# Kernel tuning notes

Hardware: AMD Instinct MI355X
Metric: run time of the kernel (lower is better)

## Reference

```python
import jax, jax.numpy as jnp
import numpy as np

B, T, C, H = 8, 1024, 1024, 16
HD = C // H  # head dim = 64
NEG = -1e9


def setup_inputs() -> dict:
    key = jax.random.key(0)
    ks = jax.random.split(key, 10)
    total = B * T
    x = jax.random.normal(ks[0], (total, C), dtype=jnp.float32)
    # identity pack: each padded row is a contiguous chunk of tokens
    padpack_index = jnp.arange(total, dtype=jnp.int64).reshape(B, T)
    # sorted per-row sequence ids -> block-diagonal attention within each packed row
    padpack_batch = jnp.sort(jax.random.randint(ks[1], (B, T), 0, 4, dtype=jnp.int32), axis=-1)
    padpack_inverse_index = jnp.arange(total, dtype=jnp.int64)
    s = 1.0 / np.sqrt(C)
    Wq = jax.random.uniform(ks[2], (C, C), jnp.float32, -s, s)
    bq = jax.random.uniform(ks[3], (C,), jnp.float32, -s, s)
    Wk = jax.random.uniform(ks[4], (C, C), jnp.float32, -s, s)
    bk = jax.random.uniform(ks[5], (C,), jnp.float32, -s, s)
    Wv = jax.random.uniform(ks[6], (C, C), jnp.float32, -s, s)
    bv = jax.random.uniform(ks[7], (C,), jnp.float32, -s, s)
    Wp = jax.random.uniform(ks[8], (C, C), jnp.float32, -s, s)
    bp = jax.random.uniform(ks[9], (C,), jnp.float32, -s, s)
    return {"x": x, "padpack_index": padpack_index, "padpack_batch": padpack_batch,
            "padpack_inverse_index": padpack_inverse_index,
            "Wq": Wq, "bq": bq, "Wk": Wk, "bk": bk, "Wv": Wv, "bv": bv, "Wp": Wp, "bp": bp}


def reference(x, padpack_index, padpack_batch, padpack_inverse_index,
              Wq, bq, Wk, bk, Wv, bv, Wp, bp):
    # gather ragged tokens into padded [B, T, C]
    xp = x[padpack_index]
    # torch Linear: y = x @ W.T + b
    q = (xp @ Wq.T + bq).reshape(B, T, H, HD)
    k = (xp @ Wk.T + bk).reshape(B, T, H, HD)
    v = (xp @ Wv.T + bv).reshape(B, T, H, HD)
    scale = 1.0 / np.sqrt(HD).astype(np.float32)
    att = jnp.einsum('bihd,bjhd->bhij', q, k) * scale  # [B,H,T,T]
    # mask: token pairs from different packed sequences cannot attend
    mask = (padpack_batch[:, :, None] != padpack_batch[:, None, :])[:, None]  # [B,1,T,T]
    att = jnp.where(mask, NEG, att)
    att = jax.nn.softmax(att, axis=-1)
    y = jnp.einsum('bhij,bjhd->bihd', att, v).reshape(B, T, C)
    y = y @ Wp.T + bp
    # scatter back to ragged layout [total_tokens, C]
    return y.reshape(B * T, C)[padpack_inverse_index]
```

## Files before the change

### kernel.cpp

```cpp
#include <hip/hip_runtime.h>


typedef __attribute__((ext_vector_type(8))) short short8;
typedef __attribute__((ext_vector_type(4))) float f32x4;

#define MFMA16(a, b, c) __builtin_amdgcn_mfma_f32_16x16x32_bf16((a), (b), (c), 0, 0, 0)

__device__ __forceinline__ ushort f2b(float f) {
  union { float f; unsigned u; } v; v.f = f;
  unsigned u = v.u;
  return (ushort)((u + 0x7fffu + ((u >> 16) & 1u)) >> 16);
}

__device__ __forceinline__ void gload16(const void* g, void* l) {
  __builtin_amdgcn_global_load_lds((const __attribute__((address_space(1))) unsigned int*)g,
                                   (__attribute__((address_space(3))) unsigned int*)l,
                                   16, 0, 0);
}

__device__ __forceinline__ void cvt4(const float* __restrict__ s, ushort* __restrict__ d) {
  const float4 v = *(const float4*)s;
  ushort4 r; r.x = f2b(v.x); r.y = f2b(v.y); r.z = f2b(v.z); r.w = f2b(v.w);
  *(ushort4*)d = r;
}

__global__ __launch_bounds__(256) void prep(const float* __restrict__ x,
    const float* __restrict__ wq, const float* __restrict__ wk,
    const float* __restrict__ wv, const float* __restrict__ wp,
    ushort* __restrict__ xb, ushort* __restrict__ wb) {
  const long long e0 = ((long long)blockIdx.x * 256 + threadIdx.x) * 4;
  const long long NX = 8388608ll;
  if (e0 < NX) {
    cvt4(x + e0, xb + e0);
  } else {
    const long long t = e0 - NX;
    const int sel = (int)(t >> 20);
    const float* w = sel == 0 ? wq : sel == 1 ? wk : sel == 2 ? wv : wp;
    cvt4(w + (t & 1048575), wb + t);
  }
}

__global__ void seg_bounds(const int* __restrict__ pb, int* __restrict__ bnd) {
  const int b = blockIdx.x, i = threadIdx.x;
  const int* p = pb + b * 1024;
  const int cur = p[i];
  const int prev = (i == 0) ? -1 : p[i - 1];
  for (int v = prev + 1; v <= cur; ++v) bnd[b * 8 + v] = i;
  if (i == 1023)
    for (int v = cur + 1; v <= 4; ++v) bnd[b * 8 + v] = 1024;
}

template <int MODE>
__global__ __launch_bounds__(512, 2) void gemm8(
    const ushort* __restrict__ A, const ushort* __restrict__ Bw,
    const float* __restrict__ bias0, const float* __restrict__ bias1,
    const float* __restrict__ bias2,
    ushort* __restrict__ O0, ushort* __restrict__ O1, ushort* __restrict__ O2,
    float* __restrict__ Of) {
  constexpr int ACH = 256 * 64;
  constexpr int BCH = 128 * 64;
  constexpr int BUFB = 2 * (ACH + BCH);
  __shared__ __align__(16) char smem[3 * BUFB];

  const int tid = threadIdx.x, lane = tid & 63, wid = tid >> 6;
  const int wr = wid >> 1, wc = wid & 1;
  const int lg = lane >> 4, lc = lane & 15;

  const int id = blockIdx.x;
  const int s = id >> 3;
  const int m0 = ((id & 7) * 4 + (s & 3)) << 8;
  const int n0 = (s >> 2) << 7;

  f32x4 acc[4][4] = {};

  const int sr0 = tid >> 2;
  const int sc0 = (tid & 3) ^ ((sr0 >> 1) & 3);

#define STAGE(dst_, kh, kt) { \
    char* ad = (dst_) + (kh) * ACH; \
    char* bd = (dst_) + 2 * ACH + (kh) * BCH; \
    const int kcol = (kt) * 64 + (kh) * 32; \
    gload16(A + (size_t)(m0 + sr0) * 1024 + kcol + sc0 * 8, ad + tid * 16); \
    gload16(A + (size_t)(m0 + 128 + sr0) * 1024 + kcol + sc0 * 8, ad + (tid + 512) * 16); \
    gload16(Bw + (size_t)(n0 + sr0) * 1024 + kcol + sc0 * 8, bd + tid * 16); \
  }

#define PHASE_COMPUTE(src_, kh) { \
    const char* ab = (src_) + (kh) * ACH; \
    const char* bb = (src_) + 2 * ACH + (kh) * BCH; \
    short8 af[4]; short8 bf[4]; \
    _Pragma("unroll") \
    for (int f = 0; f < 4; ++f) { \
      const int row = wr * 64 + f * 16 + lc; \
      af[f] = *(const short8*)(ab + row * 64 + ((lg ^ ((row >> 1) & 3)) << 4)); \
    } \
    _Pragma("unroll") \
    for (int g = 0; g < 4; ++g) { \
      const int row = wc * 64 + g * 16 + lc; \
      bf[g] = *(const short8*)(bb + row * 64 + ((lg ^ ((row >> 1) & 3)) << 4)); \
    } \
    asm volatile("s_waitcnt lgkmcnt(0)" ::: "memory"); \
    __builtin_amdgcn_sched_barrier(0); \
    __builtin_amdgcn_s_setprio(1); \
    _Pragma("unroll") \
    for (int f = 0; f < 4; ++f) \
      _Pragma("unroll") \
      for (int g = 0; g < 4; ++g) \
        acc[f][g] = MFMA16(af[f], bf[g], acc[f][g]); \
    __builtin_amdgcn_s_setprio(0); \
  }

#define WAITVM(n) { asm volatile("s_waitcnt vmcnt(" #n ")" ::: "memory"); }

  char* b0 = smem;
  char* b1 = smem + BUFB;
  char* b2 = smem + 2 * BUFB;

  STAGE(b0, 0, 0)
  STAGE(b0, 1, 0)
  STAGE(b1, 0, 1)
  STAGE(b1, 1, 1)

  for (int t = 0; t < 14; ++t) {
    WAITVM(9)
    __builtin_amdgcn_s_barrier();
    __builtin_amdgcn_sched_barrier(0);
    STAGE(b2, 0, t + 2)
    PHASE_COMPUTE(b0, 0)
    WAITVM(9)
    __builtin_amdgcn_s_barrier();
    __builtin_amdgcn_sched_barrier(0);
    STAGE(b2, 1, t + 2)
    PHASE_COMPUTE(b0, 1)
    char* tmp = b0; b0 = b1; b1 = b2; b2 = tmp;
  }
  WAITVM(9)
  __builtin_amdgcn_s_barrier();
  __builtin_amdgcn_sched_barrier(0);
  PHASE_COMPUTE(b0, 0)
  WAITVM(6)
  __builtin_amdgcn_s_barrier();
  __builtin_amdgcn_sched_barrier(0);
  PHASE_COMPUTE(b0, 1)
  WAITVM(3)
  __builtin_amdgcn_s_barrier();
  __builtin_amdgcn_sched_barrier(0);
  PHASE_COMPUTE(b1, 0)
  WAITVM(0)
  __builtin_amdgcn_s_barrier();
  __builtin_amdgcn_sched_barrier(0);
  PHASE_COMPUTE(b1, 1)

  if constexpr (MODE == 0) {
    const int sel = n0 >> 10, nloc = n0 & 1023;
    const float* bias = sel == 0 ? bias0 : sel == 1 ? bias1 : bias2;
    float bval[4];
#pragma unroll
    for (int g = 0; g < 4; ++g) bval[g] = bias[nloc + wc * 64 + g * 16 + lc];
    if (sel < 2) {
      ushort* dst = sel ? O1 : O0;
#pragma unroll
      for (int f = 0; f < 4; ++f)
#pragma unroll
        for (int j = 0; j < 4; ++j) {
          const size_t row = m0 + wr * 64 + f * 16 + lg * 4 + j;
#pragma unroll
          for (int g = 0; g < 4; ++g)
            dst[row * 1024 + nloc + wc * 64 + g * 16 + lc] = f2b(acc[f][g][j] + bval[g]);
        }
    } else {
      ushort (*Ts)[136] = (ushort(*)[136])smem;
#pragma unroll
      for (int mh = 0; mh < 2; ++mh) {
        __syncthreads();
        if ((wr >> 1) == mh) {
#pragma unroll
          for (int f = 0; f < 4; ++f)
#pragma unroll
            for (int g = 0; g < 4; ++g)
#pragma unroll
              for (int j = 0; j < 4; ++j)
                Ts[(wr & 1) * 64 + f * 16 + lg * 4 + j][wc * 64 + g * 16 + lc] =
                    f2b(acc[f][g][j] + bval[g]);
        }
        __syncthreads();
        const int c = tid >> 2;
        const int th = (tid & 3) * 32;
        const int gt = m0 + mh * 128;
        const int b = gt >> 10;
        const int t0 = (gt & 1023) + th;
        const int gc = nloc + c;
        ushort* dp = O2 + ((size_t)((b * 16 + (gc >> 6)) * 64 + (gc & 63))) * 1024 + t0;
#pragma unroll
        for (int gb = 0; gb < 4; ++gb) {
          short8 pk;
#pragma unroll
          for (int u = 0; u < 8; ++u) pk[u] = (short)Ts[th + gb * 8 + u][c];
          *(short8*)(dp + gb * 8) = pk;
        }
      }
    }
  } else {
    float bval[4];
#pragma unroll
    for (int g = 0; g < 4; ++g) bval[g] = bias0[n0 + wc * 64 + g * 16 + lc];
#pragma unroll
    for (int f = 0; f < 4; ++f)
#pragma unroll
      for (int j = 0; j < 4; ++j) {
        const size_t row = m0 + wr * 64 + f * 16 + lg * 4 + j;
#pragma unroll
        for (int g = 0; g < 4; ++g)
          Of[row * 1024 + n0 + wc * 64 + g * 16 + lc] = acc[f][g][j] + bval[g];
      }
  }
#undef STAGE
#undef PHASE_COMPUTE
#undef WAITVM
}

__global__ __launch_bounds__(256) void attn(const ushort* __restrict__ Q,
    const ushort* __restrict__ K, const ushort* __restrict__ Vt,
    const int* __restrict__ bnd, ushort* __restrict__ O) {
  __shared__ __align__(16) char kvbuf[2][16384];
  __shared__ __align__(16) ushort Plds[4][16][68];

  const int tid = threadIdx.x, lane = tid & 63, w = tid >> 6;
  const int lg = lane >> 4, lc = lane & 15;

  const int id = blockIdx.x;
  const int xcd = id & 7, slot = id >> 3;
  const int bh = xcd + 8 * (slot >> 4), qt = slot & 15;
  const int b = bh >> 4, h = bh & 15;
  const int q0 = qt * 64 + w * 16;

  const int* bd = bnd + b * 8;
  const int b1 = bd[1], b2 = bd[2], b3 = bd[3], b4 = bd[4];
#define SEGID(k) (((k) >= b1) + ((k) >= b2) + ((k) >= b3) + ((k) >= b4))

  const int qid = SEGID(q0 + lc);
  int klo_l = (qid > 0) ? b1 : 0;
  klo_l = (qid > 1) ? b2 : klo_l;
  klo_l = (qid > 2) ? b3 : klo_l;
  int khi_l = (qid > 0) ? b2 : b1;
  khi_l = (qid > 1) ? b3 : khi_l;
  khi_l = (qid > 2) ? b4 : khi_l;

  const int bq_lo = SEGID(qt * 64), bq_hi = SEGID(qt * 64 + 63);
  unsigned am = 0;
#pragma unroll
  for (int jt = 0; jt < 16; ++jt) {
    const int tlo = SEGID(jt * 64), thi = SEGID(jt * 64 + 63);
    if (thi >= bq_lo && tlo <= bq_hi) am |= (1u << jt);
  }

  const ushort* qp = Q + (size_t)(b * 1024 + q0 + lc) * 1024 + h * 64 + lg * 8;
  const short8 qf0 = *(const short8*)qp;
  const short8 qf1 = *(const short8*)(qp + 32);

  const int r0 = tid >> 3;
  const int c16 = (tid & 7) ^ (r0 & 7);
  const ushort* Kg0 = K + (size_t)(b * 1024 + r0) * 1024 + h * 64 + c16 * 8;
  const ushort* Kg1 = Kg0 + (size_t)32 * 1024;
  const ushort* Vg0 = Vt + (size_t)(bh * 64 + r0) * 1024 + c16 * 8;
  const ushort* Vg1 = Vg0 + (size_t)32 * 1024;

#define STAGE(bufp, j) { \
    gload16(Kg0 + (size_t)(j) * 1024, (bufp) + tid * 16); \
    gload16(Kg1 + (size_t)(j) * 1024, (bufp) + 4096 + tid * 16); \
    gload16(Vg0 + (j), (bufp) + 8192 + tid * 16); \
    gload16(Vg1 + (j), (bufp) + 12288 + tid * 16); }

#define SOFF(r, ch) ((r) * 128 + ((((ch) ^ ((r) & 7))) << 4))

  float mr = -1e30f, lr = 0.f;
  f32x4 o[4] = {};

  unsigned rem = am;
  int jc = __builtin_ctz(rem) * 64;
  rem &= rem - 1;
  STAGE(kvbuf[0], jc)
  __syncthreads();
  int cur = 0;

  for (;;) {
    int jn = -1;
    if (rem) {
      jn = __builtin_ctz(rem) * 64;
      rem &= rem - 1;
      STAGE(kvbuf[cur ^ 1], jn)
    }
    const char* bufK = kvbuf[cur];
    const char* bufV = kvbuf[cur] + 8192;

    short8 kf[8];
#pragma unroll
    for (int n = 0; n < 4; ++n) {
      const int rr = n * 16 + lc;
      kf[2 * n] = *(const short8*)(bufK + SOFF(rr, lg));
      kf[2 * n + 1] = *(const short8*)(bufK + SOFF(rr, lg + 4));
    }
    f32x4 s[4];
    __builtin_amdgcn_s_setprio(1);
#pragma unroll
    for (int n = 0; n < 4; ++n) {
      f32x4 z = {};
      z = MFMA16(kf[2 * n], qf0, z);
      s[n] = MFMA16(kf[2 * n + 1], qf1, z);
    }
    __builtin_amdgcn_s_setprio(0);

#pragma unroll
    for (int n = 0; n < 4; ++n) {
      const int kk = jc + n * 16 + lg * 4;
#pragma unroll
      for (int r = 0; r < 4; ++r) {
        const bool ok = (kk + r >= klo_l) && (kk + r < khi_l);
        s[n][r] = ok ? s[n][r] * 0.125f : -1e9f;
      }
    }

    float rm = fmaxf(fmaxf(fmaxf(s[0][0], s[0][1]), fmaxf(s[0][2], s[0][3])),
                     fmaxf(fmaxf(fmaxf(s[1][0], s[1][1]), fmaxf(s[1][2], s[1][3])),
                           fmaxf(fmaxf(fmaxf(s[2][0], s[2][1]), fmaxf(s[2][2], s[2][3])),
                                 fmaxf(fmaxf(s[3][0], s[3][1]), fmaxf(s[3][2], s[3][3])))));
    rm = fmaxf(rm, __shfl_xor(rm, 16));
    rm = fmaxf(rm, __shfl_xor(rm, 32));
    float mn = mr;
    if (!__all(rm <= mr + 8.f)) {
      mn = fmaxf(mr, rm);
      const float sf = __expf(mr - mn);
      mr = mn;
      lr *= sf;
      const float s0 = __shfl(sf, lg * 4 + 0);
      const float s1 = __shfl(sf, lg * 4 + 1);
      const float s2 = __shfl(sf, lg * 4 + 2);
      const float s3 = __shfl(sf, lg * 4 + 3);
#pragma unroll
      for (int n = 0; n < 4; ++n) {
        o[n][0] *= s0; o[n][1] *= s1; o[n][2] *= s2; o[n][3] *= s3;
      }
    }
    float rs = 0.f;
#pragma unroll
    for (int n = 0; n < 4; ++n)
#pragma unroll
      for (int r = 0; r < 4; ++r) {
        const float p = __expf(s[n][r] - mn);
        s[n][r] = p; rs += p;
      }
    rs += __shfl_xor(rs, 16);
    rs += __shfl_xor(rs, 32);
    lr += rs;

#pragma unroll
    for (int n = 0; n < 4; ++n) {
      ushort4 pk;
      pk.x = f2b(s[n][0]); pk.y = f2b(s[n][1]); pk.z = f2b(s[n][2]); pk.w = f2b(s[n][3]);
      *(ushort4*)&Plds[w][lc][n * 16 + lg * 4] = pk;
    }
    asm volatile("s_waitcnt lgkmcnt(0)" ::: "memory");
    __builtin_amdgcn_sched_barrier(0);
    const short8 p0 = *(const short8*)&Plds[w][lc][lg * 8];
    const short8 p1 = *(const short8*)&Plds[w][lc][32 + lg * 8];
    __builtin_amdgcn_sched_barrier(0);

    short8 vv[8];
#pragma unroll
    for (int n = 0; n < 4; ++n) {
      const int rr = n * 16 + lc;
      vv[2 * n] = *(const short8*)(bufV + SOFF(rr, lg));
      vv[2 * n + 1] = *(const short8*)(bufV + SOFF(rr, lg + 4));
    }
    __builtin_amdgcn_s_setprio(1);
#pragma unroll
    for (int n = 0; n < 4; ++n) {
      o[n] = MFMA16(p0, vv[2 * n], o[n]);
      o[n] = MFMA16(p1, vv[2 * n + 1], o[n]);
    }
    __builtin_amdgcn_s_setprio(0);

    if (jn < 0) break;
    __syncthreads();
    cur ^= 1;
    jc = jn;
  }

  const float linv = 1.f / lr;
  const float i0 = __shfl(linv, lg * 4 + 0);
  const float i1 = __shfl(linv, lg * 4 + 1);
  const float i2 = __shfl(linv, lg * 4 + 2);
  const float i3 = __shfl(linv, lg * 4 + 3);
#pragma unroll
  for (int n = 0; n < 4; ++n) {
    const size_t base = (size_t)(b * 1024 + q0) * 1024 + h * 64 + n * 16 + lc;
    O[base + 0 * 1024 + (size_t)lg * 4096] = f2b(o[n][0] * i0);
    O[base + 1 * 1024 + (size_t)lg * 4096] = f2b(o[n][1] * i1);
    O[base + 2 * 1024 + (size_t)lg * 4096] = f2b(o[n][2] * i2);
    O[base + 3 * 1024 + (size_t)lg * 4096] = f2b(o[n][3] * i3);
  }
#undef STAGE
#undef SOFF
#undef SEGID
}

extern "C" void kernel_launch(void* const* d_in, const int* in_sizes, int n_in,
                              void* d_out, int out_size, void* d_ws, size_t ws_size,
                              hipStream_t stream) {
  const float* x  = (const float*)d_in[0];
  const int*  pb  = (const int*)d_in[2];
  const float* Wq = (const float*)d_in[4]; const float* bq = (const float*)d_in[5];
  const float* Wk = (const float*)d_in[6]; const float* bk = (const float*)d_in[7];
  const float* Wv = (const float*)d_in[8]; const float* bv = (const float*)d_in[9];
  const float* Wp = (const float*)d_in[10]; const float* bp = (const float*)d_in[11];
  float* out = (float*)d_out;
  char* ws = (char*)d_ws;

  ushort* xb = (ushort*)ws;
  ushort* wb = (ushort*)(ws + (16u << 20));
  ushort* Qb = (ushort*)(ws + (24u << 20));
  ushort* Kb = (ushort*)(ws + (40u << 20));
  ushort* Vt = (ushort*)(ws + (56u << 20));
  int*    bnd = (int*)(ws + (72u << 20));
  ushort* Ob = xb;

  prep<<<12288, 256, 0, stream>>>(x, Wq, Wk, Wv, Wp, xb, wb);
  seg_bounds<<<8, 1024, 0, stream>>>(pb, bnd);
  gemm8<0><<<768, 512, 0, stream>>>(xb, wb, bq, bk, bv, Qb, Kb, Vt, nullptr);
  attn<<<2048, 256, 0, stream>>>(Qb, Kb, Vt, bnd, Ob);
  gemm8<1><<<256, 512, 0, stream>>>(Ob, wb + (3 << 20), bp,
                                    nullptr, nullptr, nullptr, nullptr, nullptr, out);
}
```

Before: 155.2 us.

## Add dedicated 256x256-tile QKV projection GEMM kernel with double-buffered LDS

Replaces the 256x128-tile QKV GEMM (768 blocks) with a new kernel that uses 256x256 output tiles (384 blocks), 8 waves in a 2x4 layout, each holding 8x4 MFMA accumulators. K is staged in 64-wide chunks through a double-buffered LDS pipeline using direct global-to-LDS loads, with setprio around MFMA bursts. The larger tile raises arithmetic intensity and cuts redundant A/B reloads, at the cost of more accumulator registers, 128KB LDS per block, and fewer blocks to spread across CUs. The old gemm8 is reduced to the output-projection mode only.

```diff
diff --git a/kernel.cpp b/kernel.cpp
--- a/kernel.cpp
+++ b/kernel.cpp
@@ -50,13 +50,175 @@
     for (int v = cur + 1; v <= 4; ++v) bnd[b * 8 + v] = 1024;
 }
 
+__global__ __launch_bounds__(512, 2) void gemm_qkv256(
+    const ushort* __restrict__ A, const ushort* __restrict__ Bw,
+    const float* __restrict__ bq, const float* __restrict__ bk, const float* __restrict__ bv,
+    ushort* __restrict__ Qb, ushort* __restrict__ Kb, ushort* __restrict__ Vt) {
+  constexpr int REG = 16384;
+  constexpr int BUFB = 4 * REG;
+  __shared__ __align__(16) char smem[2 * BUFB];
+
+  const int tid = threadIdx.x, lane = tid & 63, wid = tid >> 6;
+  const int wr = wid >> 2, wc = wid & 3;
+  const int lg = lane >> 4, lc = lane & 15;
+
+  const int id = blockIdx.x;
+  const int xcd = id & 7, s = id >> 3;
+  const int m0 = (xcd * 4 + (s & 3)) << 8;
+  const int n0 = (s >> 2) << 8;
+
+  f32x4 acc[8][4] = {};
+
+  const int sr = tid >> 2;
+  const int sc = (tid & 3) ^ ((sr >> 1) & 3);
+
+#define STG(bufp, reg_off, src, row_base, kcol) { \
+    gload16((src) + (size_t)((row_base) + sr) * 1024 + (kcol) + sc * 8, \
+            (bufp) + (reg_off) + tid * 16); \
+    gload16((src) + (size_t)((row_base) + 128 + sr) * 1024 + (kcol) + sc * 8, \
+            (bufp) + (reg_off) + 8192 + tid * 16); }
+
+#define RD_B(bufp, kh) { \
+    const char* bb = (bufp) + 2 * REG + (kh) * REG; \
+    _Pragma("unroll") \
+    for (int g = 0; g < 4; ++g) { \
+      const int row = wc * 64 + g * 16 + lc; \
+      bf[g] = *(const short8*)(bb + row * 64 + ((lg ^ ((row >> 1) & 3)) << 4)); \
+    } }
+
+#define RD_A(bufp, kh, mh) { \
+    const char* ab = (bufp) + (kh) * REG; \
+    _Pragma("unroll") \
+    for (int f = 0; f < 4; ++f) { \
+      const int row = wr * 128 + (mh) * 64 + f * 16 + lc; \
+      af[f] = *(const short8*)(ab + row * 64 + ((lg ^ ((row >> 1) & 3)) << 4)); \
+    } }
+
+#define DO_MFMA(mh) { \
+    asm volatile("s_waitcnt lgkmcnt(0)" ::: "memory"); \
+    __builtin_amdgcn_sched_barrier(0); \
+    __builtin_amdgcn_s_setprio(1); \
+    _Pragma("unroll") \
+    for (int f = 0; f < 4; ++f) \
+      _Pragma("unroll") \
+      for (int g = 0; g < 4; ++g) \
+        acc[(mh) * 4 + f][g] = MFMA16(af[f], bf[g], acc[(mh) * 4 + f][g]); \
+    __builtin_amdgcn_s_setprio(0); }
+
+#define BAR() { __builtin_amdgcn_s_barrier(); __builtin_amdgcn_sched_barrier(0); }
+#define WAITVM(n) { asm volatile("s_waitcnt vmcnt(" #n ")" ::: "memory"); }
+
+  char* cur = smem;
+  char* oth = smem + BUFB;
+
+  STG(cur, 0, A, m0, 0)
+  STG(cur, 2 * REG, Bw, n0, 0)
+  STG(cur, REG, A, m0, 32)
+  STG(cur, 3 * REG, Bw, n0, 32)
+
+  short8 af[4], bf[4];
+
+  for (int t = 0; t < 15; ++t) {
+    const int kn = (t + 1) * 64;
+    WAITVM(4)
+    BAR()
+    STG(oth, 0, A, m0, kn)
+    RD_B(cur, 0)
+    RD_A(cur, 0, 0)
+    DO_MFMA(0)
+    BAR()
+    STG(oth, 2 * REG, Bw, n0, kn)
+    RD_A(cur, 0, 1)
+    DO_MFMA(1)
+    WAITVM(4)
+    BAR()
+    STG(oth, REG, A, m0, kn + 32)
+    RD_B(cur, 1)
+    RD_A(cur, 1, 0)
+    DO_MFMA(0)
+    BAR()
+    STG(oth, 3 * REG, Bw, n0, kn + 32)
+    RD_A(cur, 1, 1)
+    DO_MFMA(1)
+    char* tmp = cur; cur = oth; oth = tmp;
+  }
+  WAITVM(4)
+  BAR()
+  RD_B(cur, 0)
+  RD_A(cur, 0, 0)
+  DO_MFMA(0)
+  BAR()
+  RD_A(cur, 0, 1)
+  DO_MFMA(1)
+  WAITVM(0)
+  BAR()
+  RD_B(cur, 1)
+  RD_A(cur, 1, 0)
+  DO_MFMA(0)
+  BAR()
+  RD_A(cur, 1, 1)
+  DO_MFMA(1)
+
+  const int sel = n0 >> 10, nloc = n0 & 1023;
+  const float* bias = sel == 0 ? bq : sel == 1 ? bk : bv;
+  float bval[4];
+#pragma unroll
+  for (int g = 0; g < 4; ++g) bval[g] = bias[nloc + wc * 64 + g * 16 + lc];
+
+  if (sel < 2) {
+    ushort* dst = sel ? Kb : Qb;
+#pragma unroll
+    for (int i = 0; i < 8; ++i)
+#pragma unroll
+      for (int j = 0; j < 4; ++j) {
+        const size_t row = m0 + wr * 128 + i * 16 + lg * 4 + j;
+#pragma unroll
+        for (int g = 0; g < 4; ++g)
+          dst[row * 1024 + nloc + wc * 64 + g * 16 + lc] = f2b(acc[i][g][j] + bval[g]);
+      }
+  } else {
+    ushort (*Ts)[264] = (ushort(*)[264])smem;
+#pragma unroll
+    for (int h2 = 0; h2 < 2; ++h2) {
+      __syncthreads();
+      if (wr == h2) {
+#pragma unroll
+        for (int i = 0; i < 8; ++i)
+#pragma unroll
+          for (int g = 0; g < 4; ++g)
+#pragma unroll
+            for (int j = 0; j < 4; ++j)
+              Ts[i * 16 + lg * 4 + j][wc * 64 + g * 16 + lc] = f2b(acc[i][g][j] + bval[g]);
+      }
+      __syncthreads();
+      const int c = tid >> 1;
+      const int th = (tid & 1) * 64;
+      const int gt = m0 + h2 * 128;
+      const int b = gt >> 10;
+      const int t0 = (gt & 1023) + th;
+      const int gc = nloc + c;
+      ushort* dp = Vt + ((size_t)((b * 16 + (gc >> 6)) * 64 + (gc & 63))) * 1024 + t0;
+#pragma unroll
+      for (int gb = 0; gb < 8; ++gb) {
+        short8 pk;
+#pragma unroll
+        for (int u = 0; u < 8; ++u) pk[u] = (short)Ts[th + gb * 8 + u][c];
+        *(short8*)(dp + gb * 8) = pk;
+      }
+    }
+  }
+#undef STG
+#undef RD_B
+#undef RD_A
+#undef DO_MFMA
+#undef BAR
+#undef WAITVM
+}
+
 template <int MODE>
 __global__ __launch_bounds__(512, 2) void gemm8(
     const ushort* __restrict__ A, const ushort* __restrict__ Bw,
-    const float* __restrict__ bias0, const float* __restrict__ bias1,
-    const float* __restrict__ bias2,
-    ushort* __restrict__ O0, ushort* __restrict__ O1, ushort* __restrict__ O2,
-    float* __restrict__ Of) {
+    const float* __restrict__ bias0, float* __restrict__ Of) {
   constexpr int ACH = 256 * 64;
   constexpr int BCH = 128 * 64;
   constexpr int BUFB = 2 * (ACH + BCH);
@@ -151,69 +313,18 @@
   __builtin_amdgcn_sched_barrier(0);
   PHASE_COMPUTE(b1, 1)
 
-  if constexpr (MODE == 0) {
-    const int sel = n0 >> 10, nloc = n0 & 1023;
-    const float* bias = sel == 0 ? bias0 : sel == 1 ? bias1 : bias2;
-    float bval[4];
-#pragma unroll
-    for (int g = 0; g < 4; ++g) bval[g] = bias[nloc + wc * 64 + g * 16 + lc];
-    if (sel < 2) {
-      ushort* dst = sel ? O1 : O0;
-#pragma unroll
-      for (int f = 0; f < 4; ++f)
-#pragma unroll
-        for (int j = 0; j < 4; ++j) {
-          const size_t row = m0 + wr * 64 + f * 16 + lg * 4 + j;
-#pragma unroll
-          for (int g = 0; g < 4; ++g)
-            dst[row * 1024 + nloc + wc * 64 + g * 16 + lc] = f2b(acc[f][g][j] + bval[g]);
-        }
-    } else {
-      ushort (*Ts)[136] = (ushort(*)[136])smem;
-#pragma unroll
-      for (int mh = 0; mh < 2; ++mh) {
-        __syncthreads();
-        if ((wr >> 1) == mh) {
-#pragma unroll
-          for (int f = 0; f < 4; ++f)
-#pragma unroll
-            for (int g = 0; g < 4; ++g)
-#pragma unroll
-              for (int j = 0; j < 4; ++j)
-                Ts[(wr & 1) * 64 + f * 16 + lg * 4 + j][wc * 64 + g * 16 + lc] =
-                    f2b(acc[f][g][j] + bval[g]);
-        }
-        __syncthreads();
-        const int c = tid >> 2;
-        const int th = (tid & 3) * 32;
-        const int gt = m0 + mh * 128;
-        const int b = gt >> 10;
-        const int t0 = (gt & 1023) + th;
-        const int gc = nloc + c;
-        ushort* dp = O2 + ((size_t)((b * 16 + (gc >> 6)) * 64 + (gc & 63))) * 1024 + t0;
-#pragma unroll
-        for (int gb = 0; gb < 4; ++gb) {
-          short8 pk;
-#pragma unroll
-          for (int u = 0; u < 8; ++u) pk[u] = (short)Ts[th + gb * 8 + u][c];
-          *(short8*)(dp + gb * 8) = pk;
-        }
-      }
-    }
-  } else {
-    float bval[4];
-#pragma unroll
-    for (int g = 0; g < 4; ++g) bval[g] = bias0[n0 + wc * 64 + g * 16 + lc];
-#pragma unroll
-    for (int f = 0; f < 4; ++f)
-#pragma unroll
-      for (int j = 0; j < 4; ++j) {
-        const size_t row = m0 + wr * 64 + f * 16 + lg * 4 + j;
-#pragma unroll
-        for (int g = 0; g < 4; ++g)
-          Of[row * 1024 + n0 + wc * 64 + g * 16 + lc] = acc[f][g][j] + bval[g];
-      }
-  }
+  float bval[4];
+#pragma unroll
+  for (int g = 0; g < 4; ++g) bval[g] = bias0[n0 + wc * 64 + g * 16 + lc];
+#pragma unroll
+  for (int f = 0; f < 4; ++f)
+#pragma unroll
+    for (int j = 0; j < 4; ++j) {
+      const size_t row = m0 + wr * 64 + f * 16 + lg * 4 + j;
+#pragma unroll
+      for (int g = 0; g < 4; ++g)
+        Of[row * 1024 + n0 + wc * 64 + g * 16 + lc] = acc[f][g][j] + bval[g];
+    }
 #undef STAGE
 #undef PHASE_COMPUTE
 #undef WAITVM
@@ -426,8 +537,7 @@
 
   prep<<<12288, 256, 0, stream>>>(x, Wq, Wk, Wv, Wp, xb, wb);
   seg_bounds<<<8, 1024, 0, stream>>>(pb, bnd);
-  gemm8<0><<<768, 512, 0, stream>>>(xb, wb, bq, bk, bv, Qb, Kb, Vt, nullptr);
+  gemm_qkv256<<<384, 512, 0, stream>>>(xb, wb, bq, bk, bv, Qb, Kb, Vt);
   attn<<<2048, 256, 0, stream>>>(Qb, Kb, Vt, bnd, Ob);
-  gemm8<1><<<256, 512, 0, stream>>>(Ob, wb + (3 << 20), bp,
-                                    nullptr, nullptr, nullptr, nullptr, nullptr, out);
-}
+  gemm8<1><<<256, 512, 0, stream>>>(Ob, wb + (3 << 20), bp, out);
+}
```

New measurement: 156.8 us. Within noise of the previous version (+1.0%).

## Fuse segment-bounds into prep kernel and widen attention blocks to 128 queries

Applied to the files above, without the earlier changes.

The separate seg_bounds launch is folded into the prep conversion kernel as 8 extra blocks, removing one kernel launch. The attention kernel goes from 256 to 512 threads per block, covering 128 query rows with 8 waves. Each staged K/V tile is now shared by twice as many waves, so redundant K/V loads are halved and each thread issues one load per tensor instead of two. In exchange, the wider query tile makes the active-key mask coarser, so blocks may process more masked key tiles, and the larger blocks may lower occupancy.

```diff
diff --git a/kernel.cpp b/kernel.cpp
--- a/kernel.cpp
+++ b/kernel.cpp
@@ -27,8 +27,27 @@
 __global__ __launch_bounds__(256) void prep(const float* __restrict__ x,
     const float* __restrict__ wq, const float* __restrict__ wk,
     const float* __restrict__ wv, const float* __restrict__ wp,
-    ushort* __restrict__ xb, ushort* __restrict__ wb) {
-  const long long e0 = ((long long)blockIdx.x * 256 + threadIdx.x) * 4;
+    ushort* __restrict__ xb, ushort* __restrict__ wb,
+    const int* __restrict__ pb, int* __restrict__ bnd) {
+  const int bid = blockIdx.x;
+  if (bid >= 12288) {
+    const int b = bid - 12288;
+    const int* p = pb + b * 1024;
+    const int i = threadIdx.x;
+#pragma unroll
+    for (int e = 0; e < 4; ++e) {
+      const int idx = i * 4 + e;
+      const int cur = p[idx];
+      const int prev = (idx == 0) ? -1 : p[idx - 1];
+      for (int v = prev + 1; v <= cur; ++v) bnd[b * 8 + v] = idx;
+    }
+    if (i == 255) {
+      const int cur = p[1023];
+      for (int v = cur + 1; v <= 4; ++v) bnd[b * 8 + v] = 1024;
+    }
+    return;
+  }
+  const long long e0 = ((long long)bid * 256 + threadIdx.x) * 4;
   const long long NX = 8388608ll;
   if (e0 < NX) {
     cvt4(x + e0, xb + e0);
@@ -38,16 +57,6 @@
     const float* w = sel == 0 ? wq : sel == 1 ? wk : sel == 2 ? wv : wp;
     cvt4(w + (t & 1048575), wb + t);
   }
-}
-
-__global__ void seg_bounds(const int* __restrict__ pb, int* __restrict__ bnd) {
-  const int b = blockIdx.x, i = threadIdx.x;
-  const int* p = pb + b * 1024;
-  const int cur = p[i];
-  const int prev = (i == 0) ? -1 : p[i - 1];
-  for (int v = prev + 1; v <= cur; ++v) bnd[b * 8 + v] = i;
-  if (i == 1023)
-    for (int v = cur + 1; v <= 4; ++v) bnd[b * 8 + v] = 1024;
 }
 
 template <int MODE>
@@ -219,20 +228,21 @@
 #undef WAITVM
 }
 
-__global__ __launch_bounds__(256) void attn(const ushort* __restrict__ Q,
+__global__ __launch_bounds__(512) void attn(const ushort* __restrict__ Q,
     const ushort* __restrict__ K, const ushort* __restrict__ Vt,
     const int* __restrict__ bnd, ushort* __restrict__ O) {
   __shared__ __align__(16) char kvbuf[2][16384];
-  __shared__ __align__(16) ushort Plds[4][16][68];
+  __shared__ __align__(16) ushort Plds[8][16][68];
 
   const int tid = threadIdx.x, lane = tid & 63, w = tid >> 6;
   const int lg = lane >> 4, lc = lane & 15;
 
   const int id = blockIdx.x;
   const int xcd = id & 7, slot = id >> 3;
-  const int bh = xcd + 8 * (slot >> 4), qt = slot & 15;
+  const int bh = xcd + 8 * (slot >> 3);
+  const int qt = slot & 7;
   const int b = bh >> 4, h = bh & 15;
-  const int q0 = qt * 64 + w * 16;
+  const int q0 = qt * 128 + w * 16;
 
   const int* bd = bnd + b * 8;
   const int b1 = bd[1], b2 = bd[2], b3 = bd[3], b4 = bd[4];
@@ -246,7 +256,7 @@
   khi_l = (qid > 1) ? b3 : khi_l;
   khi_l = (qid > 2) ? b4 : khi_l;
 
-  const int bq_lo = SEGID(qt * 64), bq_hi = SEGID(qt * 64 + 63);
+  const int bq_lo = SEGID(qt * 128), bq_hi = SEGID(qt * 128 + 127);
   unsigned am = 0;
 #pragma unroll
   for (int jt = 0; jt < 16; ++jt) {
@@ -260,16 +270,12 @@
 
   const int r0 = tid >> 3;
   const int c16 = (tid & 7) ^ (r0 & 7);
-  const ushort* Kg0 = K + (size_t)(b * 1024 + r0) * 1024 + h * 64 + c16 * 8;
-  const ushort* Kg1 = Kg0 + (size_t)32 * 1024;
-  const ushort* Vg0 = Vt + (size_t)(bh * 64 + r0) * 1024 + c16 * 8;
-  const ushort* Vg1 = Vg0 + (size_t)32 * 1024;
+  const ushort* Kg = K + (size_t)(b * 1024 + r0) * 1024 + h * 64 + c16 * 8;
+  const ushort* Vg = Vt + (size_t)(bh * 64 + r0) * 1024 + c16 * 8;
 
 #define STAGE(bufp, j) { \
-    gload16(Kg0 + (size_t)(j) * 1024, (bufp) + tid * 16); \
-    gload16(Kg1 + (size_t)(j) * 1024, (bufp) + 4096 + tid * 16); \
-    gload16(Vg0 + (j), (bufp) + 8192 + tid * 16); \
-    gload16(Vg1 + (j), (bufp) + 12288 + tid * 16); }
+    gload16(Kg + (size_t)(j) * 1024, (bufp) + tid * 16); \
+    gload16(Vg + (j), (bufp) + 8192 + tid * 16); }
 
 #define SOFF(r, ch) ((r) * 128 + ((((ch) ^ ((r) & 7))) << 4))
 
@@ -424,10 +430,9 @@
   int*    bnd = (int*)(ws + (72u << 20));
   ushort* Ob = xb;
 
-  prep<<<12288, 256, 0, stream>>>(x, Wq, Wk, Wv, Wp, xb, wb);
-  seg_bounds<<<8, 1024, 0, stream>>>(pb, bnd);
+  prep<<<12296, 256, 0, stream>>>(x, Wq, Wk, Wv, Wp, xb, wb, pb, bnd);
   gemm8<0><<<768, 512, 0, stream>>>(xb, wb, bq, bk, bv, Qb, Kb, Vt, nullptr);
-  attn<<<2048, 256, 0, stream>>>(Qb, Kb, Vt, bnd, Ob);
+  attn<<<1024, 512, 0, stream>>>(Qb, Kb, Vt, bnd, Ob);
   gemm8<1><<<256, 512, 0, stream>>>(Ob, wb + (3 << 20), bp,
                                     nullptr, nullptr, nullptr, nullptr, nullptr, out);
 }
```

New measurement: 149.0 us. -4.0%, faster.
